# Performance work log

Hardware: AMD Instinct MI355X
Metric: run time of the kernel (lower is better)

The kernel has to match this reference:

```python
import jax, jax.numpy as jnp
import numpy as np

D_MODEL = 512
NUM_HEADS = 8
DEPTH = D_MODEL // NUM_HEADS


def setup_inputs() -> dict:
    key = jax.random.key(0)
    ks = jax.random.split(key, 12)
    B, S, D = 2, 4096, D_MODEL
    scale = 1.0 / np.sqrt(D)
    return {
        "q": jax.random.normal(ks[0], (B, S, D), jnp.float32),
        "k": jax.random.normal(ks[1], (B, S, D), jnp.float32),
        "v": jax.random.normal(ks[2], (B, S, D), jnp.float32),
        "mask": jnp.zeros((B, 1, 1, S), jnp.float32),
        "wq": jax.random.normal(ks[3], (D, D), jnp.float32) * scale,
        "bq": jnp.zeros((D,), jnp.float32),
        "wk": jax.random.normal(ks[4], (D, D), jnp.float32) * scale,
        "bk": jnp.zeros((D,), jnp.float32),
        "wv": jax.random.normal(ks[5], (D, D), jnp.float32) * scale,
        "bv": jnp.zeros((D,), jnp.float32),
        "wo": jax.random.normal(ks[6], (D, D), jnp.float32) * scale,
        "bo": jnp.zeros((D,), jnp.float32),
    }


def _split_heads(x):
    # [B, S, D] -> [B, H, S, depth]
    B, S, _ = x.shape
    return x.reshape(B, S, NUM_HEADS, DEPTH).transpose(0, 2, 1, 3)


def reference(q, k, v, mask, wq, bq, wk, bk, wv, bv, wo, bo):
    B, S, D = q.shape
    query = _split_heads(q @ wq + bq)   # [B,H,S,d]
    key = _split_heads(k @ wk + bk)
    value = _split_heads(v @ wv + bv)
    # NOTE: original module does NOT scale by 1/sqrt(depth)
    score = jnp.einsum("bhqd,bhkd->bhqk", query, key)
    score = score + mask * -1e9
    attn = jax.nn.softmax(score, axis=-1)
    out = jnp.einsum("bhqk,bhkd->bhqd", attn, value)  # [B,H,S,d]
    out = out.transpose(0, 2, 1, 3).reshape(B, S, D)
    return out @ wo + bo
```

## Files before the change

### kernel.cpp

```cpp
#include <hip/hip_runtime.h>

#define NH   8
#define DH   64
#define NB   2
#define SEQ  4096
#define DM   512
#define MR   (NB * SEQ)
#define LSTR 72
#define LOG2E 1.44269504089f

using f16x8 = __attribute__((ext_vector_type(8))) _Float16;
using f32x4 = __attribute__((ext_vector_type(4))) float;
#define MFMA16(a, b, c) __builtin_amdgcn_mfma_f32_16x16x32_f16(a, b, c, 0, 0, 0)

#if defined(__has_builtin) && __has_builtin(__builtin_amdgcn_exp2f)
#define EXP2(x) __builtin_amdgcn_exp2f(x)
#else
extern "C" __device__ float __ocml_native_exp2_f32(float);
#define EXP2(x) __ocml_native_exp2_f32(x)
#endif

__device__ __forceinline__ unsigned pk_f16(float a, float b) {
    typedef __fp16 fp16v2 __attribute__((ext_vector_type(2)));
    union { fp16v2 h; unsigned u; } c;
    c.h = __builtin_amdgcn_cvt_pkrtz(a, b);
    return c.u;
}
__device__ __forceinline__ unsigned sel_shfl(unsigned a, unsigned b, int pick, int src) {
    const unsigned va = __shfl(a, src);
    const unsigned vb = __shfl(b, src);
    return pick ? vb : va;
}
__device__ __forceinline__ void async16(void* lds, const void* g) {
    __builtin_amdgcn_global_load_lds(
        (__attribute__((address_space(1))) void*)g,
        (__attribute__((address_space(3))) void*)lds, 16, 0, 0);
}

__global__ __launch_bounds__(256) void cvt_w(
    const float* __restrict__ w0, const float* __restrict__ w1,
    const float* __restrict__ w2, const float* __restrict__ w3,
    _Float16* __restrict__ Wt)
{
    __shared__ _Float16 T[64 * LSTR];
    const int z = blockIdx.z;
    const float* W = (z == 0) ? w0 : (z == 1 ? w1 : (z == 2 ? w2 : w3));
    _Float16* out = Wt + (size_t)z * DM * DM;
    const int t = threadIdx.x;
    const int k0 = blockIdx.x * 64, n0 = blockIdx.y * 64;
#pragma unroll
    for (int i = 0; i < 4; ++i) {
        const int kl  = i * 16 + (t >> 4);
        const int nl4 = (t & 15) * 4;
        float4 u = *(const float4*)(W + (size_t)(k0 + kl) * DM + n0 + nl4);
        T[(nl4 + 0) * LSTR + kl] = (_Float16)u.x;
        T[(nl4 + 1) * LSTR + kl] = (_Float16)u.y;
        T[(nl4 + 2) * LSTR + kl] = (_Float16)u.z;
        T[(nl4 + 3) * LSTR + kl] = (_Float16)u.w;
    }
    __syncthreads();
#pragma unroll
    for (int i = 0; i < 2; ++i) {
        const int nl = i * 32 + (t >> 3);
        const int kc = (t & 7) * 8;
        *(uint4*)(out + (size_t)(n0 + nl) * DM + k0 + kc) = *(const uint4*)&T[nl * LSTR + kc];
    }
}

__global__ __launch_bounds__(256) void maskprep(const float* __restrict__ mask,
                                                float* __restrict__ mw)
{
    const int i = blockIdx.x * 256 + threadIdx.x;
    mw[i] = mask[i] * (-1e9f * LOG2E);
}

__global__ __launch_bounds__(256) void cvt_qkv(
    const float* __restrict__ q, const float* __restrict__ k,
    const float* __restrict__ v,
    _Float16* __restrict__ Qo, _Float16* __restrict__ Ko, _Float16* __restrict__ Vo)
{
    const size_t PER = (size_t)MR * DM;
    size_t base = ((size_t)blockIdx.x * 256 + threadIdx.x) * 8;
    const int tz = (int)(base / PER);
    const size_t off = base % PER;
    const float* s = (tz == 0) ? q : (tz == 1 ? k : v);
    _Float16* d    = (tz == 0) ? Qo : (tz == 1 ? Ko : Vo);
    float4 a = *(const float4*)(s + off);
    float4 b = *(const float4*)(s + off + 4);
    uint4 p = make_uint4(pk_f16(a.x, a.y), pk_f16(a.z, a.w),
                         pk_f16(b.x, b.y), pk_f16(b.z, b.w));
    *(uint4*)(d + off) = p;
}

__global__ __launch_bounds__(256) void proj3(
    const _Float16* __restrict__ Qin, const _Float16* __restrict__ Kin,
    const _Float16* __restrict__ Vin, const _Float16* __restrict__ Wt,
    const float* __restrict__ bq, const float* __restrict__ bk,
    const float* __restrict__ bv,
    _Float16* __restrict__ Qo, _Float16* __restrict__ Ko,
    _Float16* __restrict__ VTo)
{
    __shared__ _Float16 Xs[2][128 * 64];
    __shared__ _Float16 Ws[2][64 * 64];

    const int z = blockIdx.z;
    const _Float16* X = (z == 0) ? Qin : (z == 1 ? Kin : Vin);
    const _Float16* W = Wt + (size_t)z * DM * DM;
    const float* bias = (z == 0) ? bq : (z == 1 ? bk : bv);
    const float scale = (z == 0) ? LOG2E : 1.0f;

    const int t = threadIdx.x;
    const int l = t & 63, w = t >> 6;
    const int m = l & 15, g = l >> 4;
    const int ms = m & 7;
    const int row0 = blockIdx.x * 128;
    const int col0 = blockIdx.y * 64;

    int xr[4], xsw[4];
#pragma unroll
    for (int i = 0; i < 4; ++i) {
        const int c = w * 256 + i * 64 + l;
        xr[i]  = c >> 3;
        xsw[i] = ((c & 7) ^ (xr[i] & 7)) * 8;
    }
    int wr[2], wsw[2];
#pragma unroll
    for (int i = 0; i < 2; ++i) {
        const int c = w * 128 + i * 64 + l;
        wr[i]  = c >> 3;
        wsw[i] = ((c & 7) ^ (wr[i] & 7)) * 8;
    }

#pragma unroll
    for (int i = 0; i < 4; ++i)
        async16(&Xs[0][(w * 256 + i * 64) * 8], X + (size_t)(row0 + xr[i]) * DM + xsw[i]);
#pragma unroll
    for (int i = 0; i < 2; ++i)
        async16(&Ws[0][(w * 128 + i * 64) * 8], W + (size_t)(col0 + wr[i]) * DM + wsw[i]);

    f32x4 acc[2][4] = {};

    for (int k0 = 0; k0 < DM; k0 += 64) {
        const int p = (k0 >> 6) & 1;
        __syncthreads();
        if (k0 + 64 < DM) {
            const int kn = k0 + 64;
#pragma unroll
            for (int i = 0; i < 4; ++i)
                async16(&Xs[p ^ 1][(w * 256 + i * 64) * 8],
                        X + (size_t)(row0 + xr[i]) * DM + kn + xsw[i]);
#pragma unroll
            for (int i = 0; i < 2; ++i)
                async16(&Ws[p ^ 1][(w * 128 + i * 64) * 8],
                        W + (size_t)(col0 + wr[i]) * DM + kn + wsw[i]);
        }
#pragma unroll
        for (int kk = 0; kk < 2; ++kk) {
            const int slot = ((kk * 4 + g) ^ ms) * 8;
            f16x8 a0 = *(const f16x8*)&Xs[p][(w * 32 + m) * 64 + slot];
            f16x8 a1 = *(const f16x8*)&Xs[p][(w * 32 + 16 + m) * 64 + slot];
#pragma unroll
            for (int ct = 0; ct < 4; ++ct) {
                f16x8 bf = *(const f16x8*)&Ws[p][(ct * 16 + m) * 64 + slot];
                acc[0][ct] = MFMA16(a0, bf, acc[0][ct]);
                acc[1][ct] = MFMA16(a1, bf, acc[1][ct]);
            }
        }
    }

    float bv4[4];
#pragma unroll
    for (int ct = 0; ct < 4; ++ct) bv4[ct] = bias[col0 + ct * 16 + m];

    if (z == 2) {
        __syncthreads();
        _Float16* T = &Xs[0][0];
#pragma unroll
        for (int rt = 0; rt < 2; ++rt)
#pragma unroll
            for (int reg = 0; reg < 4; ++reg) {
                const int s_l = w * 32 + rt * 16 + g * 4 + reg;
#pragma unroll
                for (int ct = 0; ct < 4; ++ct) {
                    const int d = ct * 16 + m;
                    T[d * 136 + s_l] = (_Float16)(acc[rt][ct][reg] + bv4[ct]);
                }
            }
        __syncthreads();
        const int bb = row0 >> 12;
        const int s0 = row0 & (SEQ - 1);
#pragma unroll
        for (int j = 0; j < 4; ++j) {
            const int c = j * 256 + t;
            const int d = c >> 4;
            const int sc = (c & 15) * 8;
            *(uint4*)(VTo + (((size_t)bb * NH + blockIdx.y) * DH + d) * SEQ + s0 + sc) =
                *(const uint4*)&T[d * 136 + sc];
        }
    } else {
        _Float16* out = (z == 0) ? Qo : Ko;
#pragma unroll
        for (int rt = 0; rt < 2; ++rt)
#pragma unroll
            for (int reg = 0; reg < 4; ++reg) {
                const int row = row0 + w * 32 + rt * 16 + g * 4 + reg;
                const int bb = row >> 12;
                const int s  = row & (SEQ - 1);
#pragma unroll
                for (int ct = 0; ct < 4; ++ct)
                    out[(((size_t)bb * NH + blockIdx.y) * SEQ + s) * DH + ct * 16 + m] =
                        (_Float16)(scale * (acc[rt][ct][reg] + bv4[ct]));
            }
    }
}

__global__ __launch_bounds__(256) void gemm_out(const _Float16* __restrict__ X,
                                                const _Float16* __restrict__ W,
                                                const float* __restrict__ bias,
                                                float* __restrict__ out)
{
    __shared__ _Float16 Xs[2][128 * 64];
    __shared__ _Float16 Ws[2][64 * 64];

    const int t = threadIdx.x;
    const int l = t & 63, w = t >> 6;
    const int m = l & 15, g = l >> 4;
    const int ms = m & 7;
    const int row0 = blockIdx.x * 128;
    const int col0 = blockIdx.y * 64;

    int xr[4], xsw[4];
#pragma unroll
    for (int i = 0; i < 4; ++i) {
        const int c = w * 256 + i * 64 + l;
        xr[i]  = c >> 3;
        xsw[i] = ((c & 7) ^ (xr[i] & 7)) * 8;
    }
    int wr[2], wsw[2];
#pragma unroll
    for (int i = 0; i < 2; ++i) {
        const int c = w * 128 + i * 64 + l;
        wr[i]  = c >> 3;
        wsw[i] = ((c & 7) ^ (wr[i] & 7)) * 8;
    }

#pragma unroll
    for (int i = 0; i < 4; ++i)
        async16(&Xs[0][(w * 256 + i * 64) * 8], X + (size_t)(row0 + xr[i]) * DM + xsw[i]);
#pragma unroll
    for (int i = 0; i < 2; ++i)
        async16(&Ws[0][(w * 128 + i * 64) * 8], W + (size_t)(col0 + wr[i]) * DM + wsw[i]);

    f32x4 acc[2][4] = {};

    for (int k0 = 0; k0 < DM; k0 += 64) {
        const int p = (k0 >> 6) & 1;
        __syncthreads();
        if (k0 + 64 < DM) {
            const int kn = k0 + 64;
#pragma unroll
            for (int i = 0; i < 4; ++i)
                async16(&Xs[p ^ 1][(w * 256 + i * 64) * 8],
                        X + (size_t)(row0 + xr[i]) * DM + kn + xsw[i]);
#pragma unroll
            for (int i = 0; i < 2; ++i)
                async16(&Ws[p ^ 1][(w * 128 + i * 64) * 8],
                        W + (size_t)(col0 + wr[i]) * DM + kn + wsw[i]);
        }
#pragma unroll
        for (int kk = 0; kk < 2; ++kk) {
            const int slot = ((kk * 4 + g) ^ ms) * 8;
            f16x8 a0 = *(const f16x8*)&Xs[p][(w * 32 + m) * 64 + slot];
            f16x8 a1 = *(const f16x8*)&Xs[p][(w * 32 + 16 + m) * 64 + slot];
#pragma unroll
            for (int ct = 0; ct < 4; ++ct) {
                f16x8 bf = *(const f16x8*)&Ws[p][(ct * 16 + m) * 64 + slot];
                acc[0][ct] = MFMA16(a0, bf, acc[0][ct]);
                acc[1][ct] = MFMA16(a1, bf, acc[1][ct]);
            }
        }
    }

    float bv4[4];
#pragma unroll
    for (int ct = 0; ct < 4; ++ct) bv4[ct] = bias[col0 + ct * 16 + m];

#pragma unroll
    for (int rt = 0; rt < 2; ++rt)
#pragma unroll
        for (int reg = 0; reg < 4; ++reg) {
            const int row = row0 + w * 32 + rt * 16 + g * 4 + reg;
#pragma unroll
            for (int ct = 0; ct < 4; ++ct)
                out[(size_t)row * DM + col0 + ct * 16 + m] = acc[rt][ct][reg] + bv4[ct];
        }
}

__global__ __launch_bounds__(256) void flash_mfma(
    const _Float16* __restrict__ Q, const _Float16* __restrict__ K,
    const _Float16* __restrict__ VT, const float* __restrict__ mw,
    _Float16* __restrict__ O)
{
    __shared__ _Float16 Ks [2][64 * 64];
    __shared__ _Float16 VTs[2][64 * 64];

    const int t = threadIdx.x;
    const int l = t & 63, w = t >> 6;
    const int m = l & 15, g = l >> 4;
    const int bh = blockIdx.y;
    const int b  = bh >> 3;
    const int h  = bh & 7;
    const int q0 = blockIdx.x * 64;

    const _Float16* Qh  = Q  + (size_t)bh * SEQ * DH;
    const _Float16* Kh  = K  + (size_t)bh * SEQ * DH;
    const _Float16* VTh = VT + (size_t)bh * DH * SEQ;
    const float* mwb = mw + (size_t)b * SEQ;

    const int c0 = w * 128 + l, c1 = c0 + 64;
    const int r0 = c0 >> 3,     r1 = c1 >> 3;
    const int cl0 = (c0 & 7) ^ (r0 & 7), cl1 = (c1 & 7) ^ (r1 & 7);
    const int    gK0 = r0 * DH + cl0 * 8, gK1 = r1 * DH + cl1 * 8;
    const size_t gV0 = (size_t)r0 * SEQ + cl0 * 8, gV1 = (size_t)r1 * SEQ + cl1 * 8;
    const int ldsA = w * 1024, ldsB = ldsA + 512;

    async16(&Ks[0][ldsA], Kh + gK0);
    async16(&Ks[0][ldsB], Kh + gK1);
    async16(&VTs[0][ldsA], VTh + gV0);
    async16(&VTs[0][ldsB], VTh + gV1);

    f16x8 qf[2];
#pragma unroll
    for (int kk = 0; kk < 2; ++kk)
        qf[kk] = *(const f16x8*)(Qh + (size_t)(q0 + w * 16 + m) * DH + kk * 32 + g * 8);

    float m_r = -INFINITY, l_r = 0.f;
    f32x4 oacc[4] = {};

    const int srcA = m + (((g * 2) & 3) << 4);
    const int srcB = m + (((g * 2 + 1) & 3) << 4);
    const int pick = g >> 1;
    const int ms = m & 7;

    for (int t0 = 0; t0 < SEQ; t0 += 64) {
        const int p = (t0 >> 6) & 1;
        __syncthreads();

        if (t0 + 64 < SEQ) {
            const int tn = t0 + 64;
            async16(&Ks[p ^ 1][ldsA], Kh + (size_t)tn * DH + gK0);
            async16(&Ks[p ^ 1][ldsB], Kh + (size_t)tn * DH + gK1);
            async16(&VTs[p ^ 1][ldsA], VTh + tn + gV0);
            async16(&VTs[p ^ 1][ldsB], VTh + tn + gV1);
        }

        f32x4 sacc[4];
#pragma unroll
        for (int kt = 0; kt < 4; ++kt)
            sacc[kt] = *(const f32x4*)&mwb[t0 + kt * 16 + g * 4];
#pragma unroll
        for (int kk = 0; kk < 2; ++kk) {
            const int slot = ((kk * 4 + g) ^ ms) * 8;
#pragma unroll
            for (int kt = 0; kt < 4; ++kt) {
                f16x8 kf = *(const f16x8*)&Ks[p][(kt * 16 + m) * 64 + slot];
                sacc[kt] = MFMA16(kf, qf[kk], sacc[kt]);
            }
        }

        float rmax = -INFINITY;
#pragma unroll
        for (int kt = 0; kt < 4; ++kt)
            rmax = fmaxf(rmax, fmaxf(fmaxf(sacc[kt][0], sacc[kt][1]),
                                     fmaxf(sacc[kt][2], sacc[kt][3])));
        rmax = fmaxf(rmax, __shfl_xor(rmax, 16));
        rmax = fmaxf(rmax, __shfl_xor(rmax, 32));
        const float mnew  = fmaxf(m_r, rmax);
        const float alpha = EXP2(m_r - mnew);
        m_r = mnew;

        float psum = 0.f;
        unsigned pkw[4][2];
#pragma unroll
        for (int kt = 0; kt < 4; ++kt) {
            const float p0 = EXP2(sacc[kt][0] - mnew);
            const float p1 = EXP2(sacc[kt][1] - mnew);
            const float p2 = EXP2(sacc[kt][2] - mnew);
            const float p3 = EXP2(sacc[kt][3] - mnew);
            psum += (p0 + p1) + (p2 + p3);
            pkw[kt][0] = pk_f16(p0, p1);
            pkw[kt][1] = pk_f16(p2, p3);
        }
        l_r = l_r * alpha + psum;
#pragma unroll
        for (int dt = 0; dt < 4; ++dt)
#pragma unroll
            for (int r = 0; r < 4; ++r) oacc[dt][r] *= alpha;

#pragma unroll
        for (int kk = 0; kk < 2; ++kk) {
            union { unsigned u[4]; f16x8 h; } pf;
            pf.u[0] = sel_shfl(pkw[2 * kk][0], pkw[2 * kk + 1][0], pick, srcA);
            pf.u[1] = sel_shfl(pkw[2 * kk][1], pkw[2 * kk + 1][1], pick, srcA);
            pf.u[2] = sel_shfl(pkw[2 * kk][0], pkw[2 * kk + 1][0], pick, srcB);
            pf.u[3] = sel_shfl(pkw[2 * kk][1], pkw[2 * kk + 1][1], pick, srcB);
            const int slot = ((kk * 4 + g) ^ ms) * 8;
#pragma unroll
            for (int dt = 0; dt < 4; ++dt) {
                f16x8 vf = *(const f16x8*)&VTs[p][(dt * 16 + m) * 64 + slot];
                oacc[dt] = MFMA16(vf, pf.h, oacc[dt]);
            }
        }
    }

    l_r += __shfl_xor(l_r, 16);
    l_r += __shfl_xor(l_r, 32);
    const float inv = 1.0f / l_r;
    const int q = q0 + w * 16 + m;
    _Float16* Orow = O + ((size_t)b * SEQ + q) * DM + h * DH;
#pragma unroll
    for (int dt = 0; dt < 4; ++dt) {
        _Float16 o4[4] = { (_Float16)(oacc[dt][0] * inv), (_Float16)(oacc[dt][1] * inv),
                           (_Float16)(oacc[dt][2] * inv), (_Float16)(oacc[dt][3] * inv) };
        *(uint2*)(Orow + dt * 16 + g * 4) = *(const uint2*)o4;
    }
}

extern "C" void kernel_launch(void* const* d_in, const int* in_sizes, int n_in,
                              void* d_out, int out_size, void* d_ws, size_t ws_size,
                              hipStream_t stream) {
    const float* q    = (const float*)d_in[0];
    const float* k    = (const float*)d_in[1];
    const float* v    = (const float*)d_in[2];
    const float* mask = (const float*)d_in[3];
    const float* wq   = (const float*)d_in[4];
    const float* bq   = (const float*)d_in[5];
    const float* wk   = (const float*)d_in[6];
    const float* bk   = (const float*)d_in[7];
    const float* wv   = (const float*)d_in[8];
    const float* bv   = (const float*)d_in[9];
    const float* wo   = (const float*)d_in[10];
    const float* bo   = (const float*)d_in[11];

    const size_t P8 = (size_t)MR * DM;
    _Float16* Wt  = (_Float16*)d_ws;
    float*    mw  = (float*)(Wt + (size_t)4 * DM * DM);
    _Float16* Qin = (_Float16*)(mw + NB * SEQ);
    _Float16* Kin = Qin + P8;
    _Float16* Vin = Kin + P8;
    _Float16* Qws = Vin + P8;
    _Float16* Kws = Qws + P8;
    _Float16* VTws = Kws + P8;
    _Float16* Ows  = VTws + P8;

    cvt_w<<<dim3(8, 8, 4), 256, 0, stream>>>(wq, wk, wv, wo, Wt);
    maskprep<<<dim3(NB * SEQ / 256), 256, 0, stream>>>(mask, mw);
    cvt_qkv<<<dim3(3 * (MR * DM / 8) / 256), 256, 0, stream>>>(q, k, v, Qin, Kin, Vin);

    proj3<<<dim3(MR / 128, DM / 64, 3), 256, 0, stream>>>(
        Qin, Kin, Vin, Wt, bq, bk, bv, Qws, Kws, VTws);

    flash_mfma<<<dim3(SEQ / 64, NB * NH), 256, 0, stream>>>(Qws, Kws, VTws, mw, Ows);

    gemm_out<<<dim3(MR / 128, DM / 64), 256, 0, stream>>>(
        Ows, Wt + (size_t)3 * DM * DM, bo, (float*)d_out);
}
```

Measured before the change: 290.9 us.

## Split attention KV range across two blocks, skip rescale lazily, combine partials

Splits the flash attention key/value sequence into two halves processed by separate blocks (grid z dimension) that write fp16 partial outputs plus per-row max and sum, then merges them in a new combine kernel. This doubles the number of blocks from 1024 to 2048 for more parallelism per launch. It also adds a lazy rescale that only updates the running max when it grows by more than 8 (in log2 units), and computes the row sum with fdot2 on the packed fp16 probabilities. The cost is an extra kernel launch, extra partial-result traffic, and an fp16 rounding of the partials before the merge.

After: 287.2 us. Within noise of the previous version (-1.3%).

```diff
diff --git a/kernel.cpp b/kernel.cpp
--- a/kernel.cpp
+++ b/kernel.cpp
@@ -8,9 +8,13 @@
 #define MR   (NB * SEQ)
 #define LSTR 72
 #define LOG2E 1.44269504089f
+#define NSPL 2
+#define KVS  (SEQ / NSPL)
+#define RH   (NB * NH * SEQ)
 
 using f16x8 = __attribute__((ext_vector_type(8))) _Float16;
 using f32x4 = __attribute__((ext_vector_type(4))) float;
+using h2    = __attribute__((ext_vector_type(2))) _Float16;
 #define MFMA16(a, b, c) __builtin_amdgcn_mfma_f32_16x16x32_f16(a, b, c, 0, 0, 0)
 
 #if defined(__has_builtin) && __has_builtin(__builtin_amdgcn_exp2f)
@@ -30,6 +34,19 @@
     const unsigned va = __shfl(a, src);
     const unsigned vb = __shfl(b, src);
     return pick ? vb : va;
+}
+__device__ __forceinline__ float m3(float a, float b, float c) {
+    return fmaxf(fmaxf(a, b), c);
+}
+__device__ __forceinline__ float dot2acc(unsigned u, float c) {
+#if defined(__has_builtin) && __has_builtin(__builtin_amdgcn_fdot2)
+    h2 a = __builtin_bit_cast(h2, u);
+    h2 one = {(_Float16)1.f, (_Float16)1.f};
+    return __builtin_amdgcn_fdot2(a, one, c, false);
+#else
+    h2 a = __builtin_bit_cast(h2, u);
+    return c + (float)a[0] + (float)a[1];
+#endif
 }
 __device__ __forceinline__ void async16(void* lds, const void* g) {
     __builtin_amdgcn_global_load_lds(
@@ -299,7 +316,7 @@
 __global__ __launch_bounds__(256) void flash_mfma(
     const _Float16* __restrict__ Q, const _Float16* __restrict__ K,
     const _Float16* __restrict__ VT, const float* __restrict__ mw,
-    _Float16* __restrict__ O)
+    _Float16* __restrict__ Op, float* __restrict__ Ml)
 {
     __shared__ _Float16 Ks [2][64 * 64];
     __shared__ _Float16 VTs[2][64 * 64];
@@ -309,8 +326,9 @@
     const int m = l & 15, g = l >> 4;
     const int bh = blockIdx.y;
     const int b  = bh >> 3;
-    const int h  = bh & 7;
     const int q0 = blockIdx.x * 64;
+    const int z  = blockIdx.z;
+    const int kb0 = z * KVS;
 
     const _Float16* Qh  = Q  + (size_t)bh * SEQ * DH;
     const _Float16* Kh  = K  + (size_t)bh * SEQ * DH;
@@ -324,10 +342,10 @@
     const size_t gV0 = (size_t)r0 * SEQ + cl0 * 8, gV1 = (size_t)r1 * SEQ + cl1 * 8;
     const int ldsA = w * 1024, ldsB = ldsA + 512;
 
-    async16(&Ks[0][ldsA], Kh + gK0);
-    async16(&Ks[0][ldsB], Kh + gK1);
-    async16(&VTs[0][ldsA], VTh + gV0);
-    async16(&VTs[0][ldsB], VTh + gV1);
+    async16(&Ks[0][ldsA], Kh + (size_t)kb0 * DH + gK0);
+    async16(&Ks[0][ldsB], Kh + (size_t)kb0 * DH + gK1);
+    async16(&VTs[0][ldsA], VTh + kb0 + gV0);
+    async16(&VTs[0][ldsB], VTh + kb0 + gV1);
 
     f16x8 qf[2];
 #pragma unroll
@@ -342,11 +360,12 @@
     const int pick = g >> 1;
     const int ms = m & 7;
 
-    for (int t0 = 0; t0 < SEQ; t0 += 64) {
-        const int p = (t0 >> 6) & 1;
+    for (int it = 0; it < KVS / 64; ++it) {
+        const int t0 = kb0 + it * 64;
+        const int p  = it & 1;
         __syncthreads();
 
-        if (t0 + 64 < SEQ) {
+        if (it + 1 < KVS / 64) {
             const int tn = t0 + 64;
             async16(&Ks[p ^ 1][ldsA], Kh + (size_t)tn * DH + gK0);
             async16(&Ks[p ^ 1][ldsB], Kh + (size_t)tn * DH + gK1);
@@ -368,34 +387,45 @@
             }
         }
 
-        float rmax = -INFINITY;
-#pragma unroll
-        for (int kt = 0; kt < 4; ++kt)
-            rmax = fmaxf(rmax, fmaxf(fmaxf(sacc[kt][0], sacc[kt][1]),
-                                     fmaxf(sacc[kt][2], sacc[kt][3])));
+        const float x0 = m3(sacc[0][0], sacc[0][1], sacc[0][2]);
+        const float x1 = m3(sacc[0][3], sacc[1][0], sacc[1][1]);
+        const float x2 = m3(sacc[1][2], sacc[1][3], sacc[2][0]);
+        const float x3 = m3(sacc[2][1], sacc[2][2], sacc[2][3]);
+        const float x4 = m3(sacc[3][0], sacc[3][1], sacc[3][2]);
+        float rmax = fmaxf(m3(x0, x1, x2), m3(x3, x4, sacc[3][3]));
         rmax = fmaxf(rmax, __shfl_xor(rmax, 16));
         rmax = fmaxf(rmax, __shfl_xor(rmax, 32));
-        const float mnew  = fmaxf(m_r, rmax);
-        const float alpha = EXP2(m_r - mnew);
-        m_r = mnew;
-
-        float psum = 0.f;
+
+        if (!__all(rmax <= m_r + 8.f)) {
+            const float mnew  = fmaxf(m_r, rmax);
+            const float alpha = EXP2(m_r - mnew);
+            m_r = mnew;
+            l_r *= alpha;
+#pragma unroll
+            for (int dt = 0; dt < 4; ++dt)
+#pragma unroll
+                for (int r = 0; r < 4; ++r) oacc[dt][r] *= alpha;
+        }
+
+        float ps0 = 0.f, ps1 = 0.f;
         unsigned pkw[4][2];
 #pragma unroll
         for (int kt = 0; kt < 4; ++kt) {
-            const float p0 = EXP2(sacc[kt][0] - mnew);
-            const float p1 = EXP2(sacc[kt][1] - mnew);
-            const float p2 = EXP2(sacc[kt][2] - mnew);
-            const float p3 = EXP2(sacc[kt][3] - mnew);
-            psum += (p0 + p1) + (p2 + p3);
+            const float p0 = EXP2(sacc[kt][0] - m_r);
+            const float p1 = EXP2(sacc[kt][1] - m_r);
+            const float p2 = EXP2(sacc[kt][2] - m_r);
+            const float p3 = EXP2(sacc[kt][3] - m_r);
             pkw[kt][0] = pk_f16(p0, p1);
             pkw[kt][1] = pk_f16(p2, p3);
-        }
-        l_r = l_r * alpha + psum;
-#pragma unroll
-        for (int dt = 0; dt < 4; ++dt)
-#pragma unroll
-            for (int r = 0; r < 4; ++r) oacc[dt][r] *= alpha;
+            if (kt < 2) {
+                ps0 = dot2acc(pkw[kt][0], ps0);
+                ps0 = dot2acc(pkw[kt][1], ps0);
+            } else {
+                ps1 = dot2acc(pkw[kt][0], ps1);
+                ps1 = dot2acc(pkw[kt][1], ps1);
+            }
+        }
+        l_r += ps0 + ps1;
 
 #pragma unroll
         for (int kk = 0; kk < 2; ++kk) {
@@ -417,13 +447,40 @@
     l_r += __shfl_xor(l_r, 32);
     const float inv = 1.0f / l_r;
     const int q = q0 + w * 16 + m;
-    _Float16* Orow = O + ((size_t)b * SEQ + q) * DM + h * DH;
+    const size_t rowi = ((size_t)z * NB * NH + bh) * SEQ + q;
+    _Float16* Orow = Op + rowi * DH;
 #pragma unroll
     for (int dt = 0; dt < 4; ++dt) {
         _Float16 o4[4] = { (_Float16)(oacc[dt][0] * inv), (_Float16)(oacc[dt][1] * inv),
                            (_Float16)(oacc[dt][2] * inv), (_Float16)(oacc[dt][3] * inv) };
         *(uint2*)(Orow + dt * 16 + g * 4) = *(const uint2*)o4;
     }
+    if (g == 0) ((float2*)Ml)[rowi] = make_float2(m_r, l_r);
+}
+
+__global__ __launch_bounds__(256) void combine(const _Float16* __restrict__ Op,
+                                               const float* __restrict__ Ml,
+                                               _Float16* __restrict__ O)
+{
+    const int i = blockIdx.x * 256 + threadIdx.x;
+    const int r = i >> 4;
+    const int dq = (i & 15) * 4;
+    const float2 ml0 = ((const float2*)Ml)[r];
+    const float2 ml1 = ((const float2*)Ml)[RH + r];
+    const float M = fmaxf(ml0.x, ml1.x);
+    float a0 = EXP2(ml0.x - M) * ml0.y;
+    float a1 = EXP2(ml1.x - M) * ml1.y;
+    const float inv = 1.f / (a0 + a1);
+    a0 *= inv; a1 *= inv;
+    union { uint2 u; _Float16 h[4]; } v0, v1, o;
+    v0.u = *(const uint2*)(Op + (size_t)r * DH + dq);
+    v1.u = *(const uint2*)(Op + ((size_t)RH + r) * DH + dq);
+#pragma unroll
+    for (int j = 0; j < 4; ++j)
+        o.h[j] = (_Float16)(a0 * (float)v0.h[j] + a1 * (float)v1.h[j]);
+    const int bh = r >> 12, q = r & (SEQ - 1);
+    const int b = bh >> 3, h = bh & 7;
+    *(uint2*)(O + ((size_t)b * SEQ + q) * DM + h * DH + dq) = o.u;
 }
 
 extern "C" void kernel_launch(void* const* d_in, const int* in_sizes, int n_in,
@@ -453,6 +510,9 @@
     _Float16* VTws = Kws + P8;
     _Float16* Ows  = VTws + P8;
 
+    _Float16* Opart = Qin;
+    float*    Mlb   = (float*)Vin;
+
     cvt_w<<<dim3(8, 8, 4), 256, 0, stream>>>(wq, wk, wv, wo, Wt);
     maskprep<<<dim3(NB * SEQ / 256), 256, 0, stream>>>(mask, mw);
     cvt_qkv<<<dim3(3 * (MR * DM / 8) / 256), 256, 0, stream>>>(q, k, v, Qin, Kin, Vin);
@@ -460,7 +520,10 @@
     proj3<<<dim3(MR / 128, DM / 64, 3), 256, 0, stream>>>(
         Qin, Kin, Vin, Wt, bq, bk, bv, Qws, Kws, VTws);
 
-    flash_mfma<<<dim3(SEQ / 64, NB * NH), 256, 0, stream>>>(Qws, Kws, VTws, mw, Ows);
+    flash_mfma<<<dim3(SEQ / 64, NB * NH, NSPL), 256, 0, stream>>>(
+        Qws, Kws, VTws, mw, Opart, Mlb);
+
+    combine<<<dim3(RH * 16 / 256), 256, 0, stream>>>(Opart, Mlb, Ows);
 
     gemm_out<<<dim3(MR / 128, DM / 64), 256, 0, stream>>>(
         Ows, Wt + (size_t)3 * DM * DM, bo, (float*)d_out);
```
